# Kernel tuning notes

Measured on AMD Instinct MI355X. Metric: run time of the kernel, lower is better.

Reference implementation:

```python
import jax, jax.numpy as jnp
import numpy as np

B, O, M, H, E = 32, 64, 128, 4, 64  # batch, num_obj, memory_len, heads, embed


def setup_inputs() -> dict:
    key = jax.random.key(0)
    ks = jax.random.split(key, 10)
    s = 1.0 / np.sqrt(E)
    return {
        "query": jax.random.normal(ks[0], (B, O, E), jnp.float32),
        "context": jax.random.normal(ks[1], (B, M, E), jnp.float32),
        "memory": jax.random.normal(ks[2], (B, M, E), jnp.float32),
        "W_ch": jax.random.normal(ks[3], (E, H * E), jnp.float32) * s,
        "b_ch": jax.random.normal(ks[4], (H * E,), jnp.float32) * s,
        "w_logit": jax.random.normal(ks[5], (E,), jnp.float32) * s,
        "b_logit": jax.random.normal(ks[6], (1,), jnp.float32) * s,
        "W_rh": jax.random.normal(ks[7], (H * E, E), jnp.float32) * (1.0 / np.sqrt(H * E)),
        "b_rh": jax.random.normal(ks[8], (E,), jnp.float32) * (1.0 / np.sqrt(H * E)),
        "temp": jnp.float32(1.0),
    }


def reference(query, context, memory, W_ch, b_ch, w_logit, b_logit, W_rh, b_rh, temp):
    # create heads: [B,O,E] -> [B,O,H,E]
    q = (query @ W_ch + b_ch).reshape(B, O, H, E)
    # broadcast add query heads and context over memory axis: [B,O,M,H,E]
    qc = jnp.tanh(context[:, None, :, None, :] + q[:, :, None, :, :])
    # logit projection -> [B,O,M,H]
    logits = jnp.einsum("bomhe,e->bomh", qc, w_logit) + b_logit[0]
    # softmax over memory axis (dim=2)
    probs = jax.nn.softmax(logits / temp, axis=2)
    # weighted sum of memory over M: [B,O,H,E]
    heads = jnp.einsum("bomh,bme->bohe", probs, memory)
    heads = jax.nn.leaky_relu(heads, negative_slope=0.01)
    out = heads.reshape(B, O, H * E) @ W_rh + b_rh
    return out
```

## Files before the change

### kernel.cpp

```cpp
#include <hip/hip_runtime.h>
#include <hip/hip_fp16.h>

#define B 32
#define O 64
#define M 128
#define H 4
#define E 64
#define SC 2.88539008177792681f
#define LOG2E 1.44269504088896341f

#if __has_builtin(__builtin_amdgcn_exp2f)
#define EXP2F(x) __builtin_amdgcn_exp2f(x)
#else
#define EXP2F(x) __exp2f(x)
#endif

__device__ __forceinline__ unsigned pk2h(float a, float b) {
    return (unsigned)__half_as_ushort(__float2half_rn(a)) |
           ((unsigned)__half_as_ushort(__float2half_rn(b)) << 16);
}

__global__ __launch_bounds__(256) void prep_kernel(
    const float* __restrict__ query, const float* __restrict__ context,
    const float* __restrict__ memory, const float* __restrict__ W_ch,
    const float* __restrict__ b_ch,
    __half* __restrict__ ctx_Eh, __half* __restrict__ mem_T, float* __restrict__ q_E)
{
    __shared__ float s[128 * 68];
    const int t = threadIdx.x, blk = blockIdx.x;

    if (blk < 32) {
        const int b = blk;
        const int e = t >> 2, mb = (t & 3) * 32;
        const float* ctx = context + b * (M * E);
        #pragma unroll
        for (int i = 0; i < 8; ++i) {
            int idx = i * 1024 + t * 4;
            float4 v = *(const float4*)(ctx + idx);
            *(float4*)(&s[(idx >> 6) * 68 + (idx & 63)]) = v;
        }
        __syncthreads();
        {
            uint4* dst = (uint4*)(ctx_Eh + (size_t)b * (E * M) + e * M + mb);
            #pragma unroll
            for (int qd = 0; qd < 4; ++qd) {
                unsigned u[4];
                #pragma unroll
                for (int k = 0; k < 4; ++k) {
                    int m0 = mb + qd * 8 + 2 * k;
                    float ea = fminf(EXP2F(SC * s[m0 * 68 + e]), 60000.f);
                    float eb = fminf(EXP2F(SC * s[(m0 + 1) * 68 + e]), 60000.f);
                    u[k] = pk2h(ea, eb);
                }
                dst[qd] = make_uint4(u[0], u[1], u[2], u[3]);
            }
        }
        __syncthreads();
        const float* mem = memory + b * (M * E);
        #pragma unroll
        for (int i = 0; i < 8; ++i) {
            int idx = i * 1024 + t * 4;
            float4 v = *(const float4*)(mem + idx);
            *(float4*)(&s[(idx >> 6) * 68 + (idx & 63)]) = v;
        }
        __syncthreads();
        {
            uint4* dst = (uint4*)(mem_T + (size_t)b * (E * M) + e * M + mb);
            #pragma unroll
            for (int qd = 0; qd < 4; ++qd) {
                unsigned u[4];
                #pragma unroll
                for (int k = 0; k < 4; ++k) {
                    int m0 = mb + qd * 8 + 2 * k;
                    u[k] = pk2h(s[m0 * 68 + e], s[(m0 + 1) * 68 + e]);
                }
                dst[qd] = make_uint4(u[0], u[1], u[2], u[3]);
            }
        }
    } else {
        const int r0 = (blk - 32) * 4;
        s[t] = query[(r0 + (t & 3)) * 64 + (t >> 2)];
        __syncthreads();
        float bc = b_ch[t];
        float a0 = bc, a1 = bc, a2 = bc, a3 = bc;
        #pragma unroll 8
        for (int k = 0; k < 64; ++k) {
            float4 qv = *(const float4*)(&s[k * 4]);
            float wv = W_ch[k * 256 + t];
            a0 = fmaf(qv.x, wv, a0);
            a1 = fmaf(qv.y, wv, a1);
            a2 = fmaf(qv.z, wv, a2);
            a3 = fmaf(qv.w, wv, a3);
        }
        float* qa = q_E + (size_t)r0 * 256 + t;
        qa[0]   = EXP2F(SC * a0);
        qa[256] = EXP2F(SC * a1);
        qa[512] = EXP2F(SC * a2);
        qa[768] = EXP2F(SC * a3);
    }
}

__global__ __launch_bounds__(256) void attn_main(
    const __half* __restrict__ ctx_Eh, const __half* __restrict__ mem_T,
    const float* __restrict__ q_E, const float* __restrict__ w_logit,
    const float* __restrict__ b_logit, const float* __restrict__ temp,
    __half* __restrict__ heads_h)
{
    __shared__ __half s_E[E * M];
    __shared__ float4 s_qwu[H * E];
    __shared__ float  s_prob0[M * H];
    __shared__ float  s_prob1[M * H];
    __shared__ float  s_part0[H * 4 * E];
    __shared__ float  s_part1[H * 4 * E];

    const int t = threadIdx.x, lane = t & 63, w = t >> 6;
    const int bo0 = blockIdx.x * 2, bo1 = bo0 + 1, b = bo0 >> 6;

    {
        const uint4* g = (const uint4*)(ctx_Eh + (size_t)b * (E * M));
        uint4* l = (uint4*)s_E;
        #pragma unroll
        for (int p = 0; p < 4; ++p)
            l[p * 256 + t] = g[p * 256 + t];
    }
    const float wl = w_logit[lane];
    s_qwu[t] = make_float4(wl, q_E[bo0 * 256 + t], q_E[bo1 * 256 + t], 0.f);
    float sumw = wl;
    #pragma unroll
    for (int sft = 1; sft < 64; sft <<= 1) sumw += __shfl_xor(sumw, sft);
    const float bl   = b_logit[0];
    const float lsc  = LOG2E / temp[0];
    const float base = (sumw + bl) * lsc;
    const float lsc2 = -2.0f * lsc;
    __syncthreads();

    float a00 = 0.f, a01 = 0.f, a10 = 0.f, a11 = 0.f;
    const __half2* Ep = (const __half2*)s_E;
    const float4*  qp = &s_qwu[w * 64];
    #pragma unroll 4
    for (int e = 0; e < 64; ++e) {
        float2 cf = __half22float2(Ep[e * 64 + lane]);
        float4 qw = qp[e];
        float t00 = fmaf(cf.x, qw.y, 1.0f);
        float t01 = fmaf(cf.y, qw.y, 1.0f);
        float t10 = fmaf(cf.x, qw.z, 1.0f);
        float t11 = fmaf(cf.y, qw.z, 1.0f);
        float r0 = __builtin_amdgcn_rcpf(t00 * t01);
        float r1 = __builtin_amdgcn_rcpf(t10 * t11);
        float w0 = qw.x * r0;
        float w1 = qw.x * r1;
        a00 = fmaf(w0, t01, a00);  a01 = fmaf(w0, t00, a01);
        a10 = fmaf(w1, t11, a10);  a11 = fmaf(w1, t10, a11);
    }

    uint4 mr[4];
    {
        const uint4* mp = (const uint4*)(mem_T + (size_t)b * (E * M) + lane * M + 32 * w);
        mr[0] = mp[0]; mr[1] = mp[1]; mr[2] = mp[2]; mr[3] = mp[3];
    }

    float l00 = fmaf(lsc2, a00, base), l01 = fmaf(lsc2, a01, base);
    float l10 = fmaf(lsc2, a10, base), l11 = fmaf(lsc2, a11, base);
    float mx0 = fmaxf(l00, l01), mx1 = fmaxf(l10, l11);
    #pragma unroll
    for (int sft = 1; sft < 64; sft <<= 1) {
        mx0 = fmaxf(mx0, __shfl_xor(mx0, sft));
        mx1 = fmaxf(mx1, __shfl_xor(mx1, sft));
    }
    float e00 = EXP2F(l00 - mx0), e01 = EXP2F(l01 - mx0);
    float e10 = EXP2F(l10 - mx1), e11 = EXP2F(l11 - mx1);
    float s0 = e00 + e01, s1 = e10 + e11;
    #pragma unroll
    for (int sft = 1; sft < 64; sft <<= 1) {
        s0 += __shfl_xor(s0, sft);
        s1 += __shfl_xor(s1, sft);
    }
    float rs0 = __builtin_amdgcn_rcpf(s0), rs1 = __builtin_amdgcn_rcpf(s1);
    s_prob0[(2 * lane) * H + w]     = e00 * rs0;
    s_prob0[(2 * lane + 1) * H + w] = e01 * rs0;
    s_prob1[(2 * lane) * H + w]     = e10 * rs1;
    s_prob1[(2 * lane + 1) * H + w] = e11 * rs1;
    __syncthreads();

    float h00 = 0.f, h01 = 0.f, h02 = 0.f, h03 = 0.f;
    float h10 = 0.f, h11 = 0.f, h12 = 0.f, h13 = 0.f;
    {
        union { uint4 u4[4]; __half2 h2[16]; } mu;
        mu.u4[0] = mr[0]; mu.u4[1] = mr[1]; mu.u4[2] = mr[2]; mu.u4[3] = mr[3];
        const int mbase = 32 * w;
        #pragma unroll 8
        for (int j = 0; j < 16; ++j) {
            float2 mv = __half22float2(mu.h2[j]);
            int m = mbase + 2 * j;
            float4 pa = *(const float4*)(&s_prob0[m * 4]);
            float4 pb = *(const float4*)(&s_prob0[(m + 1) * 4]);
            h00 = fmaf(pa.x, mv.x, h00); h01 = fmaf(pa.y, mv.x, h01);
            h02 = fmaf(pa.z, mv.x, h02); h03 = fmaf(pa.w, mv.x, h03);
            h00 = fmaf(pb.x, mv.y, h00); h01 = fmaf(pb.y, mv.y, h01);
            h02 = fmaf(pb.z, mv.y, h02); h03 = fmaf(pb.w, mv.y, h03);
            float4 pc = *(const float4*)(&s_prob1[m * 4]);
            float4 pd = *(const float4*)(&s_prob1[(m + 1) * 4]);
            h10 = fmaf(pc.x, mv.x, h10); h11 = fmaf(pc.y, mv.x, h11);
            h12 = fmaf(pc.z, mv.x, h12); h13 = fmaf(pc.w, mv.x, h13);
            h10 = fmaf(pd.x, mv.y, h10); h11 = fmaf(pd.y, mv.y, h11);
            h12 = fmaf(pd.z, mv.y, h12); h13 = fmaf(pd.w, mv.y, h13);
        }
    }
    s_part0[0 * 256 + w * 64 + lane] = h00;
    s_part0[1 * 256 + w * 64 + lane] = h01;
    s_part0[2 * 256 + w * 64 + lane] = h02;
    s_part0[3 * 256 + w * 64 + lane] = h03;
    s_part1[0 * 256 + w * 64 + lane] = h10;
    s_part1[1 * 256 + w * 64 + lane] = h11;
    s_part1[2 * 256 + w * 64 + lane] = h12;
    s_part1[3 * 256 + w * 64 + lane] = h13;
    __syncthreads();
    float hv0 = s_part0[w * 256 + lane] + s_part0[w * 256 + 64 + lane]
              + s_part0[w * 256 + 128 + lane] + s_part0[w * 256 + 192 + lane];
    float hv1 = s_part1[w * 256 + lane] + s_part1[w * 256 + 64 + lane]
              + s_part1[w * 256 + 128 + lane] + s_part1[w * 256 + 192 + lane];
    hv0 = (hv0 > 0.f) ? hv0 : 0.01f * hv0;
    hv1 = (hv1 > 0.f) ? hv1 : 0.01f * hv1;
    heads_h[(size_t)bo0 * 256 + t] = __float2half_rn(hv0);
    heads_h[(size_t)bo1 * 256 + t] = __float2half_rn(hv1);
}

__global__ __launch_bounds__(256) void post_kernel(
    const __half* __restrict__ heads_h, const float* __restrict__ W_rh,
    const float* __restrict__ b_rh, float* __restrict__ out)
{
    __shared__ __half s_h[4 * 256];
    const int t = threadIdx.x, lane = t & 63, r = t >> 6;
    const int r0 = blockIdx.x * 4;
    ((uint4*)s_h)[t & 127] = ((const uint4*)(heads_h + (size_t)r0 * 256))[t & 127];
    __syncthreads();
    const __half2* hr = (const __half2*)(s_h + r * 256);
    const float* Wp = W_rh + lane;
    float acc = 0.f;
    #pragma unroll 8
    for (int jp = 0; jp < 128; ++jp) {
        float2 hh = __half22float2(hr[jp]);
        acc = fmaf(hh.x, Wp[(2 * jp) * 64], acc);
        acc = fmaf(hh.y, Wp[(2 * jp + 1) * 64], acc);
    }
    out[(size_t)(r0 + r) * 64 + lane] = acc + b_rh[lane];
}

extern "C" void kernel_launch(void* const* d_in, const int* in_sizes, int n_in,
                              void* d_out, int out_size, void* d_ws, size_t ws_size,
                              hipStream_t stream) {
    const float* query   = (const float*)d_in[0];
    const float* context = (const float*)d_in[1];
    const float* memory  = (const float*)d_in[2];
    const float* W_ch    = (const float*)d_in[3];
    const float* b_ch    = (const float*)d_in[4];
    const float* w_logit = (const float*)d_in[5];
    const float* b_logit = (const float*)d_in[6];
    const float* W_rh    = (const float*)d_in[7];
    const float* b_rh    = (const float*)d_in[8];
    const float* temp    = (const float*)d_in[9];
    float* out = (float*)d_out;

    __half* ctx_Eh  = (__half*)d_ws;
    __half* mem_T   = ctx_Eh + (size_t)B * E * M;
    float*  q_E     = (float*)(mem_T + (size_t)B * E * M);
    __half* heads_h = (__half*)(q_E + (size_t)B * O * 256);

    prep_kernel<<<544, 256, 0, stream>>>(query, context, memory, W_ch, b_ch,
                                         ctx_Eh, mem_T, q_E);
    attn_main<<<B * O / 2, 256, 0, stream>>>(ctx_Eh, mem_T, q_E, w_logit,
                                             b_logit, temp, heads_h);
    post_kernel<<<512, 256, 0, stream>>>(heads_h, W_rh, b_rh, out);
}
```

Baseline: 101.8 us.

## Read context and packed query table directly from global, drop LDS staging

The prep kernel now writes a packed float4 table (w_logit, exp-query for the two objects) per block, so attn_main no longer builds s_qwu. attn_main also stops staging the context tile into shared memory and reads it from global/cache inside the logit loop. This removes a __syncthreads and about 18KB of LDS per block, which may raise occupancy. In exchange, the inner loop issues global loads that depend on L1/L2 hits, and the workspace table grows.

Result: slower. 110.2 us (+8.2%).

```diff
diff --git a/kernel.cpp b/kernel.cpp
--- a/kernel.cpp
+++ b/kernel.cpp
@@ -23,8 +23,8 @@
 __global__ __launch_bounds__(256) void prep_kernel(
     const float* __restrict__ query, const float* __restrict__ context,
     const float* __restrict__ memory, const float* __restrict__ W_ch,
-    const float* __restrict__ b_ch,
-    __half* __restrict__ ctx_Eh, __half* __restrict__ mem_T, float* __restrict__ q_E)
+    const float* __restrict__ b_ch, const float* __restrict__ w_logit,
+    __half* __restrict__ ctx_Eh, __half* __restrict__ mem_T, float4* __restrict__ qw_tab)
 {
     __shared__ float s[128 * 68];
     const int t = threadIdx.x, blk = blockIdx.x;
@@ -92,39 +92,28 @@
             a2 = fmaf(qv.z, wv, a2);
             a3 = fmaf(qv.w, wv, a3);
         }
-        float* qa = q_E + (size_t)r0 * 256 + t;
-        qa[0]   = EXP2F(SC * a0);
-        qa[256] = EXP2F(SC * a1);
-        qa[512] = EXP2F(SC * a2);
-        qa[768] = EXP2F(SC * a3);
+        const float wl = w_logit[t & 63];
+        const int p0 = r0 >> 1;
+        qw_tab[(size_t)p0 * 256 + t]       = make_float4(wl, EXP2F(SC * a0), EXP2F(SC * a1), 0.f);
+        qw_tab[(size_t)(p0 + 1) * 256 + t] = make_float4(wl, EXP2F(SC * a2), EXP2F(SC * a3), 0.f);
     }
 }
 
 __global__ __launch_bounds__(256) void attn_main(
     const __half* __restrict__ ctx_Eh, const __half* __restrict__ mem_T,
-    const float* __restrict__ q_E, const float* __restrict__ w_logit,
+    const float4* __restrict__ qw_tab, const float* __restrict__ w_logit,
     const float* __restrict__ b_logit, const float* __restrict__ temp,
     __half* __restrict__ heads_h)
 {
-    __shared__ __half s_E[E * M];
-    __shared__ float4 s_qwu[H * E];
-    __shared__ float  s_prob0[M * H];
-    __shared__ float  s_prob1[M * H];
-    __shared__ float  s_part0[H * 4 * E];
-    __shared__ float  s_part1[H * 4 * E];
+    __shared__ float s_prob0[M * H];
+    __shared__ float s_prob1[M * H];
+    __shared__ float s_part0[H * 4 * E];
+    __shared__ float s_part1[H * 4 * E];
 
     const int t = threadIdx.x, lane = t & 63, w = t >> 6;
     const int bo0 = blockIdx.x * 2, bo1 = bo0 + 1, b = bo0 >> 6;
 
-    {
-        const uint4* g = (const uint4*)(ctx_Eh + (size_t)b * (E * M));
-        uint4* l = (uint4*)s_E;
-        #pragma unroll
-        for (int p = 0; p < 4; ++p)
-            l[p * 256 + t] = g[p * 256 + t];
-    }
     const float wl = w_logit[lane];
-    s_qwu[t] = make_float4(wl, q_E[bo0 * 256 + t], q_E[bo1 * 256 + t], 0.f);
     float sumw = wl;
     #pragma unroll
     for (int sft = 1; sft < 64; sft <<= 1) sumw += __shfl_xor(sumw, sft);
@@ -132,25 +121,26 @@
     const float lsc  = LOG2E / temp[0];
     const float base = (sumw + bl) * lsc;
     const float lsc2 = -2.0f * lsc;
-    __syncthreads();
 
     float a00 = 0.f, a01 = 0.f, a10 = 0.f, a11 = 0.f;
-    const __half2* Ep = (const __half2*)s_E;
-    const float4*  qp = &s_qwu[w * 64];
-    #pragma unroll 4
-    for (int e = 0; e < 64; ++e) {
-        float2 cf = __half22float2(Ep[e * 64 + lane]);
-        float4 qw = qp[e];
-        float t00 = fmaf(cf.x, qw.y, 1.0f);
-        float t01 = fmaf(cf.y, qw.y, 1.0f);
-        float t10 = fmaf(cf.x, qw.z, 1.0f);
-        float t11 = fmaf(cf.y, qw.z, 1.0f);
-        float r0 = __builtin_amdgcn_rcpf(t00 * t01);
-        float r1 = __builtin_amdgcn_rcpf(t10 * t11);
-        float w0 = qw.x * r0;
-        float w1 = qw.x * r1;
-        a00 = fmaf(w0, t01, a00);  a01 = fmaf(w0, t00, a01);
-        a10 = fmaf(w1, t11, a10);  a11 = fmaf(w1, t10, a11);
+    {
+        const __half2* cg = (const __half2*)(ctx_Eh + (size_t)b * (E * M));
+        const float4*  qw = qw_tab + (size_t)blockIdx.x * 256 + w * 64;
+        #pragma unroll 8
+        for (int e = 0; e < 64; ++e) {
+            float2 cf = __half22float2(cg[e * 64 + lane]);
+            float4 q  = qw[e];
+            float t00 = fmaf(cf.x, q.y, 1.0f);
+            float t01 = fmaf(cf.y, q.y, 1.0f);
+            float t10 = fmaf(cf.x, q.z, 1.0f);
+            float t11 = fmaf(cf.y, q.z, 1.0f);
+            float r0 = __builtin_amdgcn_rcpf(t00 * t01);
+            float r1 = __builtin_amdgcn_rcpf(t10 * t11);
+            float w0 = q.x * r0;
+            float w1 = q.x * r1;
+            a00 = fmaf(w0, t01, a00);  a01 = fmaf(w0, t00, a01);
+            a10 = fmaf(w1, t11, a10);  a11 = fmaf(w1, t10, a11);
+        }
     }
 
     uint4 mr[4];
@@ -263,12 +253,12 @@
 
     __half* ctx_Eh  = (__half*)d_ws;
     __half* mem_T   = ctx_Eh + (size_t)B * E * M;
-    float*  q_E     = (float*)(mem_T + (size_t)B * E * M);
-    __half* heads_h = (__half*)(q_E + (size_t)B * O * 256);
+    float4* qw_tab  = (float4*)(mem_T + (size_t)B * E * M);
+    __half* heads_h = (__half*)(qw_tab + (size_t)1024 * 256);
 
     prep_kernel<<<544, 256, 0, stream>>>(query, context, memory, W_ch, b_ch,
-                                         ctx_Eh, mem_T, q_E);
-    attn_main<<<B * O / 2, 256, 0, stream>>>(ctx_Eh, mem_T, q_E, w_logit,
+                                         w_logit, ctx_Eh, mem_T, qw_tab);
+    attn_main<<<B * O / 2, 256, 0, stream>>>(ctx_Eh, mem_T, qw_tab, w_logit,
                                              b_logit, temp, heads_h);
     post_kernel<<<512, 256, 0, stream>>>(heads_h, W_rh, b_rh, out);
 }
```

## Fuse output projection into attention kernel and split prep context/memory blocks

Applied to the files above, without the earlier changes.

The separate post_kernel is removed. The W_rh projection now runs inside attn_main, using readlane to broadcast each wave's head values and a shared-memory reduction across the four waves. This drops one launch and the fp16 heads round trip through global memory, and the heads now stay in fp32. In prep_kernel, context and memory transposes go to separate blocks (64 instead of 32), which shortens the critical path of those blocks. In exchange, each attention block reads the full W_rh matrix, and 64 serial readlane steps add to its tail.

Result: faster. 99.16 us (-2.6%).

```diff
diff --git a/kernel.cpp b/kernel.cpp
--- a/kernel.cpp
+++ b/kernel.cpp
@@ -15,6 +15,9 @@
 #define EXP2F(x) __exp2f(x)
 #endif
 
+__device__ __forceinline__ float rl(float v, int lane) {
+    return __uint_as_float(__builtin_amdgcn_readlane(__float_as_uint(v), lane));
+}
 __device__ __forceinline__ unsigned pk2h(float a, float b) {
     return (unsigned)__half_as_ushort(__float2half_rn(a)) |
            ((unsigned)__half_as_ushort(__float2half_rn(b)) << 16);
@@ -29,18 +32,19 @@
     __shared__ float s[128 * 68];
     const int t = threadIdx.x, blk = blockIdx.x;
 
-    if (blk < 32) {
-        const int b = blk;
+    if (blk < 64) {
+        const int b = blk & 31;
+        const bool is_ctx = blk < 32;
         const int e = t >> 2, mb = (t & 3) * 32;
-        const float* ctx = context + b * (M * E);
+        const float* src = (is_ctx ? context : memory) + b * (M * E);
         #pragma unroll
         for (int i = 0; i < 8; ++i) {
             int idx = i * 1024 + t * 4;
-            float4 v = *(const float4*)(ctx + idx);
+            float4 v = *(const float4*)(src + idx);
             *(float4*)(&s[(idx >> 6) * 68 + (idx & 63)]) = v;
         }
         __syncthreads();
-        {
+        if (is_ctx) {
             uint4* dst = (uint4*)(ctx_Eh + (size_t)b * (E * M) + e * M + mb);
             #pragma unroll
             for (int qd = 0; qd < 4; ++qd) {
@@ -54,17 +58,7 @@
                 }
                 dst[qd] = make_uint4(u[0], u[1], u[2], u[3]);
             }
-        }
-        __syncthreads();
-        const float* mem = memory + b * (M * E);
-        #pragma unroll
-        for (int i = 0; i < 8; ++i) {
-            int idx = i * 1024 + t * 4;
-            float4 v = *(const float4*)(mem + idx);
-            *(float4*)(&s[(idx >> 6) * 68 + (idx & 63)]) = v;
-        }
-        __syncthreads();
-        {
+        } else {
             uint4* dst = (uint4*)(mem_T + (size_t)b * (E * M) + e * M + mb);
             #pragma unroll
             for (int qd = 0; qd < 4; ++qd) {
@@ -78,7 +72,7 @@
             }
         }
     } else {
-        const int r0 = (blk - 32) * 4;
+        const int r0 = (blk - 64) * 4;
         s[t] = query[(r0 + (t & 3)) * 64 + (t >> 2)];
         __syncthreads();
         float bc = b_ch[t];
@@ -104,7 +98,8 @@
     const __half* __restrict__ ctx_Eh, const __half* __restrict__ mem_T,
     const float* __restrict__ q_E, const float* __restrict__ w_logit,
     const float* __restrict__ b_logit, const float* __restrict__ temp,
-    __half* __restrict__ heads_h)
+    const float* __restrict__ W_rh, const float* __restrict__ b_rh,
+    float* __restrict__ out)
 {
     __shared__ __half s_E[E * M];
     __shared__ float4 s_qwu[H * E];
@@ -112,6 +107,8 @@
     __shared__ float  s_prob1[M * H];
     __shared__ float  s_part0[H * 4 * E];
     __shared__ float  s_part1[H * 4 * E];
+    __shared__ float  s_po0[4 * E];
+    __shared__ float  s_po1[4 * E];
 
     const int t = threadIdx.x, lane = t & 63, w = t >> 6;
     const int bo0 = blockIdx.x * 2, bo1 = bo0 + 1, b = bo0 >> 6;
@@ -221,29 +218,30 @@
               + s_part1[w * 256 + 128 + lane] + s_part1[w * 256 + 192 + lane];
     hv0 = (hv0 > 0.f) ? hv0 : 0.01f * hv0;
     hv1 = (hv1 > 0.f) ? hv1 : 0.01f * hv1;
-    heads_h[(size_t)bo0 * 256 + t] = __float2half_rn(hv0);
-    heads_h[(size_t)bo1 * 256 + t] = __float2half_rn(hv1);
-}
-
-__global__ __launch_bounds__(256) void post_kernel(
-    const __half* __restrict__ heads_h, const float* __restrict__ W_rh,
-    const float* __restrict__ b_rh, float* __restrict__ out)
-{
-    __shared__ __half s_h[4 * 256];
-    const int t = threadIdx.x, lane = t & 63, r = t >> 6;
-    const int r0 = blockIdx.x * 4;
-    ((uint4*)s_h)[t & 127] = ((const uint4*)(heads_h + (size_t)r0 * 256))[t & 127];
-    __syncthreads();
-    const __half2* hr = (const __half2*)(s_h + r * 256);
-    const float* Wp = W_rh + lane;
-    float acc = 0.f;
-    #pragma unroll 8
-    for (int jp = 0; jp < 128; ++jp) {
-        float2 hh = __half22float2(hr[jp]);
-        acc = fmaf(hh.x, Wp[(2 * jp) * 64], acc);
-        acc = fmaf(hh.y, Wp[(2 * jp + 1) * 64], acc);
-    }
-    out[(size_t)(r0 + r) * 64 + lane] = acc + b_rh[lane];
+
+    {
+        float acc0 = 0.f, acc1 = 0.f;
+        const float* Wp = W_rh + (w * 64) * 64 + lane;
+        #pragma unroll 8
+        for (int jj = 0; jj < 64; ++jj) {
+            float wv = Wp[jj * 64];
+            float hj0 = rl(hv0, jj);
+            float hj1 = rl(hv1, jj);
+            acc0 = fmaf(hj0, wv, acc0);
+            acc1 = fmaf(hj1, wv, acc1);
+        }
+        s_po0[w * 64 + lane] = acc0;
+        s_po1[w * 64 + lane] = acc1;
+    }
+    __syncthreads();
+    if (t < 64) {
+        float o = s_po0[t] + s_po0[64 + t] + s_po0[128 + t] + s_po0[192 + t] + b_rh[t];
+        out[(size_t)bo0 * 64 + t] = o;
+    } else if (t < 128) {
+        int e2 = t - 64;
+        float o = s_po1[e2] + s_po1[64 + e2] + s_po1[128 + e2] + s_po1[192 + e2] + b_rh[e2];
+        out[(size_t)bo1 * 64 + e2] = o;
+    }
 }
 
 extern "C" void kernel_launch(void* const* d_in, const int* in_sizes, int n_in,
@@ -264,11 +262,9 @@
     __half* ctx_Eh  = (__half*)d_ws;
     __half* mem_T   = ctx_Eh + (size_t)B * E * M;
     float*  q_E     = (float*)(mem_T + (size_t)B * E * M);
-    __half* heads_h = (__half*)(q_E + (size_t)B * O * 256);
-
-    prep_kernel<<<544, 256, 0, stream>>>(query, context, memory, W_ch, b_ch,
+
+    prep_kernel<<<576, 256, 0, stream>>>(query, context, memory, W_ch, b_ch,
                                          ctx_Eh, mem_T, q_E);
     attn_main<<<B * O / 2, 256, 0, stream>>>(ctx_Eh, mem_T, q_E, w_logit,
-                                             b_logit, temp, heads_h);
-    post_kernel<<<512, 256, 0, stream>>>(heads_h, W_rh, b_rh, out);
-}
+                                             b_logit, temp, W_rh, b_rh, out);
+}
```
